# Optimization experiments

Measured on AMD Instinct MI355X. Metric: run time of the kernel, lower is better.

Reference implementation:

```python
import jax, jax.numpy as jnp
import numpy as np

N = 10000      # nodes
E = 320000     # edges (before self-loops)
IN = 256       # in_channels
HID = 128      # hidden_channels
HEADS = 4
OUT = 64       # out_channels
G = 64         # graphs in batch
NEG_SLOPE = 0.2


def setup_inputs() -> dict:
    key = jax.random.key(0)
    ks = jax.random.split(key, 12)
    s = lambda fan: 1.0 / np.sqrt(fan)
    x = jax.random.normal(ks[0], (N, IN), jnp.float32)
    edge_index = jax.random.randint(ks[1], (2, E), 0, N, dtype=jnp.int32)
    batch = jnp.sort(jax.random.randint(ks[2], (N,), 0, G, dtype=jnp.int32))
    # layer 0: GATConv(IN -> HID, heads=HEADS, concat)
    W1 = jax.random.normal(ks[3], (IN, HEADS * HID), jnp.float32) * s(IN)
    a1s = jax.random.normal(ks[4], (HEADS, HID), jnp.float32) * s(HID)
    a1d = jax.random.normal(ks[5], (HEADS, HID), jnp.float32) * s(HID)
    b1 = jnp.zeros((HEADS * HID,), jnp.float32)
    # layer 1: GATConv(HEADS*HID -> HID, heads=1)
    W2 = jax.random.normal(ks[6], (HEADS * HID, HID), jnp.float32) * s(HEADS * HID)
    a2s = jax.random.normal(ks[7], (1, HID), jnp.float32) * s(HID)
    a2d = jax.random.normal(ks[8], (1, HID), jnp.float32) * s(HID)
    b2 = jnp.zeros((HID,), jnp.float32)
    fc_w = jax.random.normal(ks[9], (HID, OUT), jnp.float32) * s(HID)
    fc_b = jnp.zeros((OUT,), jnp.float32)
    return dict(x=x, edge_index=edge_index, batch=batch, W1=W1, a1s=a1s,
                a1d=a1d, b1=b1, W2=W2, a2s=a2s, a2d=a2d, b2=b2,
                fc_w=fc_w, fc_b=fc_b)


def _gat_conv(x, src, dst, W, a_src, a_dst, b, heads):
    """PyG GATConv (concat=True, self-loops already in src/dst)."""
    n = x.shape[0]
    h = (x @ W).reshape(n, heads, -1)                     # [N,H,C]
    alpha_s = jnp.einsum('nhc,hc->nh', h, a_src)          # [N,H]
    alpha_d = jnp.einsum('nhc,hc->nh', h, a_dst)
    e = jax.nn.leaky_relu(alpha_s[src] + alpha_d[dst], NEG_SLOPE)  # [Etot,H]
    # per-destination-node segment softmax
    e = e - jax.ops.segment_max(e, dst, num_segments=n)[dst]
    e = jnp.exp(e)
    denom = jax.ops.segment_sum(e, dst, num_segments=n)[dst] + 1e-16
    alpha = e / denom
    out = jax.ops.segment_sum(h[src] * alpha[:, :, None], dst, num_segments=n)
    return out.reshape(n, -1) + b


def reference(x, edge_index, batch, W1, a1s, a1d, b1, W2, a2s, a2d, b2, fc_w, fc_b):
    loops = jnp.arange(N, dtype=edge_index.dtype)
    ei = jnp.concatenate([edge_index, jnp.stack([loops, loops])], axis=1)
    src, dst = ei[0], ei[1]
    h = jax.nn.relu(_gat_conv(x, src, dst, W1, a1s, a1d, b1, HEADS))
    h = jax.nn.relu(_gat_conv(h, src, dst, W2, a2s, a2d, b2, 1))
    # global_mean_pool over graph ids
    counts = jax.ops.segment_sum(jnp.ones((N, 1), h.dtype), batch, num_segments=G)
    pooled = jax.ops.segment_sum(h, batch, num_segments=G) / jnp.maximum(counts, 1.0)
    return pooled @ fc_w + fc_b
```

## Files before the change

### kernel.cpp

```cpp
#include <hip/hip_runtime.h>
#include <math.h>

#define NN 10000
#define EE 320000
#define GG 64
#define NT 157
#define NPAD (NT * 64)

#define NB 64
#define CH (EE / NB)
#define HSTR 10240

typedef __attribute__((ext_vector_type(8))) short short8;
typedef __attribute__((ext_vector_type(4))) float f32x4;

__device__ __forceinline__ float leaky(float x) { return x >= 0.f ? x : 0.2f * x; }

__device__ __forceinline__ unsigned f2bf(float f) {
  unsigned u = __float_as_uint(f);
  return (u + 0x7fffu + ((u >> 16) & 1u)) >> 16;
}
__device__ __forceinline__ float bflo(unsigned v) { return __uint_as_float(v << 16); }
__device__ __forceinline__ float bfhi(unsigned v) { return __uint_as_float(v & 0xffff0000u); }

__global__ __launch_bounds__(256) void zero_k(float* __restrict__ as1,
                                              float* __restrict__ ad1,
                                              float* __restrict__ as2,
                                              float* __restrict__ ad2) {
  int i = blockIdx.x * 256 + threadIdx.x;
  if (i < NN) { as2[i] = 0.f; ad2[i] = 0.f; }
  if (i < NN * 4) { as1[i] = 0.f; ad1[i] = 0.f; }
}

__device__ void histA_body(int blk, const int* __restrict__ ei,
                           int* __restrict__ hist2d,
                           ushort* __restrict__ lrank) {
  __shared__ int lh[NN];
  for (int i = threadIdx.x; i < NN; i += 256) lh[i] = 0;
  __syncthreads();
  const int base = blk * CH;
  for (int i = threadIdx.x; i < CH; i += 256) {
    int d = ei[EE + base + i];
    int r = atomicAdd(&lh[d], 1);
    lrank[base + i] = (ushort)r;
  }
  __syncthreads();
  int* hrow = hist2d + (size_t)blk * HSTR;
  for (int i = threadIdx.x; i < NN; i += 256) hrow[i] = lh[i];
}

__device__ __forceinline__ void s1_body(int sb, const int* __restrict__ hist2d,
                                        int* __restrict__ off2d,
                                        int* __restrict__ total) {
  int t = sb * 256 + threadIdx.x;
  if (t >= NN) return;
  int run = 0;
#pragma unroll 8
  for (int b = 0; b < NB; b++) {
    int v = hist2d[(size_t)b * HSTR + t];
    off2d[(size_t)b * HSTR + t] = run;
    run += v;
  }
  total[t] = run;
}

__device__ void scan_body(const int* __restrict__ total,
                          int* __restrict__ rowstart) {
  __shared__ int part[256];
  const int tid = threadIdx.x;
  const int PER = 40;
  int base = tid * PER;
  int local[PER];
  int s = 0;
#pragma unroll
  for (int i = 0; i < PER; i++) {
    int idx = base + i;
    int v = (idx < NN) ? total[idx] : 0;
    local[i] = s;
    s += v;
  }
  part[tid] = s;
  __syncthreads();
  for (int off = 1; off < 256; off <<= 1) {
    int v = (tid >= off) ? part[tid - off] : 0;
    __syncthreads();
    part[tid] += v;
    __syncthreads();
  }
  int pre = (tid == 0) ? 0 : part[tid - 1];
#pragma unroll
  for (int i = 0; i < PER; i++) {
    int idx = base + i;
    if (idx < NN) rowstart[idx] = pre + local[i];
  }
  if (tid == 255) rowstart[NN] = part[255];
}

__device__ __forceinline__ void fillB_body(int bx, const int* __restrict__ ei,
                                           const int* __restrict__ rowstart,
                                           const int* __restrict__ off2d,
                                           const ushort* __restrict__ lrank,
                                           int* __restrict__ esrc) {
  int e = bx * 256 + threadIdx.x;
  if (e >= EE) return;
  int d = ei[EE + e];
  int s = ei[e];
  int blk = e / CH;
  int pos = rowstart[d] + off2d[(size_t)blk * HSTR + d] + (int)lrank[e];
  esrc[pos] = s;
}

#define PX_ITEMS (NN * 256 / 8)
#define PW1 (512 * 256)
#define PW2 (128 * 512)
#define PACK_BLKS ((PX_ITEMS + PW1 + PW2) / 256)

__device__ __forceinline__ void pack_body(int pb, const float* __restrict__ x,
                                          const float* __restrict__ W1,
                                          const float* __restrict__ W2,
                                          uint4* __restrict__ xb,
                                          ushort* __restrict__ w1hi,
                                          ushort* __restrict__ w1lo,
                                          ushort* __restrict__ w2hi,
                                          ushort* __restrict__ w2lo) {
  int idx = pb * 256 + threadIdx.x;
  if (idx < PX_ITEMS) {
    const float4* xf = (const float4*)x;
    float4 a = xf[idx * 2], b = xf[idx * 2 + 1];
    uint4 o;
    o.x = f2bf(a.x) | (f2bf(a.y) << 16);
    o.y = f2bf(a.z) | (f2bf(a.w) << 16);
    o.z = f2bf(b.x) | (f2bf(b.y) << 16);
    o.w = f2bf(b.z) | (f2bf(b.w) << 16);
    xb[idx] = o;
  } else if (idx < PX_ITEMS + PW1) {
    int i = idx - PX_ITEMS;
    int c = i >> 8, k = i & 255;
    float w = W1[(size_t)k * 512 + c];
    unsigned h = f2bf(w);
    float r = w - __uint_as_float(h << 16);
    w1hi[i] = (ushort)h;
    w1lo[i] = (ushort)f2bf(r);
  } else if (idx < PX_ITEMS + PW1 + PW2) {
    int i = idx - PX_ITEMS - PW1;
    int c = i >> 9, k = i & 511;
    float w = W2[(size_t)k * 128 + c];
    unsigned h = f2bf(w);
    float r = w - __uint_as_float(h << 16);
    w2hi[i] = (ushort)h;
    w2lo[i] = (ushort)f2bf(r);
  }
}

__device__ __forceinline__ void gstart_body(int gb, const int* __restrict__ batch,
                                            int* __restrict__ gstart) {
  int i = gb * 256 + threadIdx.x;
  if (i >= NN) return;
  int b = batch[i];
  int prev = (i == 0) ? -1 : batch[i - 1];
  for (int g = prev + 1; g <= b; g++) gstart[g] = i;
  if (i == NN - 1)
    for (int g = b + 1; g <= GG; g++) gstart[g] = NN;
}

__device__ void gemmt_body(int chblk, int nodeblk,
                           const ushort* __restrict__ ab,
                           const ushort* __restrict__ whi,
                           const ushort* __restrict__ wlo,
                           unsigned* __restrict__ op,
                           const float* __restrict__ avs,
                           const float* __restrict__ avd,
                           float* __restrict__ as_out,
                           float* __restrict__ ad_out,
                           int K, int C) {
  const int lane = threadIdx.x & 63;
  const int wave = threadIdx.x >> 6;
  const int l15 = lane & 15;
  const int kg = lane >> 4;
  const int ch0 = chblk * 64 + wave * 16;
  const int node0 = nodeblk * 64;
  const ushort* arow_hi = whi + (size_t)(ch0 + l15) * K + kg * 8;
  const ushort* arow_lo = wlo + (size_t)(ch0 + l15) * K + kg * 8;
  const ushort* brow = ab + (size_t)(node0 + l15) * K + kg * 8;
  f32x4 acc[4];
#pragma unroll
  for (int f = 0; f < 4; f++) acc[f] = (f32x4){0.f, 0.f, 0.f, 0.f};
  for (int k0 = 0; k0 < K; k0 += 32) {
    short8 ah = *(const short8*)(arow_hi + k0);
    short8 al = *(const short8*)(arow_lo + k0);
#pragma unroll
    for (int f = 0; f < 4; f++) {
      short8 bv = *(const short8*)(brow + (size_t)f * 16 * K + k0);
      acc[f] = __builtin_amdgcn_mfma_f32_16x16x32_bf16(ah, bv, acc[f], 0, 0, 0);
      acc[f] = __builtin_amdgcn_mfma_f32_16x16x32_bf16(al, bv, acc[f], 0, 0, 0);
    }
  }
  const int chw = ch0 + kg * 4;
  const int head = ch0 >> 7;
  const int H = C >> 7;
  const float4 s4 = *(const float4*)(avs + chw);
  const float4 d4 = *(const float4*)(avd + chw);
#pragma unroll
  for (int f = 0; f < 4; f++) {
    int node = node0 + f * 16 + l15;
    unsigned u0 = f2bf(acc[f][0]) | (f2bf(acc[f][1]) << 16);
    unsigned u1 = f2bf(acc[f][2]) | (f2bf(acc[f][3]) << 16);
    *(uint2*)(op + (size_t)node * (C >> 1) + (chw >> 1)) = make_uint2(u0, u1);
    float ss = acc[f][0] * s4.x + acc[f][1] * s4.y + acc[f][2] * s4.z + acc[f][3] * s4.w;
    float sd = acc[f][0] * d4.x + acc[f][1] * d4.y + acc[f][2] * d4.z + acc[f][3] * d4.w;
    ss += __shfl_xor(ss, 16, 64); ss += __shfl_xor(ss, 32, 64);
    sd += __shfl_xor(sd, 16, 64); sd += __shfl_xor(sd, 32, 64);
    if (kg == 0 && node < NN) {
      atomicAdd(&as_out[node * H + head], ss);
      atomicAdd(&ad_out[node * H + head], sd);
    }
  }
}

#define FILL_BLKS 1250
#define GST_BLKS 40
__global__ __launch_bounds__(256) void fusedA_k(const int* __restrict__ ei,
                                                int* __restrict__ hist2d,
                                                ushort* __restrict__ lrank,
                                                const float* __restrict__ x,
                                                const float* __restrict__ W1,
                                                const float* __restrict__ W2,
                                                uint4* __restrict__ xb,
                                                ushort* __restrict__ w1hi,
                                                ushort* __restrict__ w1lo,
                                                ushort* __restrict__ w2hi,
                                                ushort* __restrict__ w2lo,
                                                const int* __restrict__ batch,
                                                int* __restrict__ gstart) {
  int bx = blockIdx.x;
  if (bx < NB) histA_body(bx, ei, hist2d, lrank);
  else if (bx < NB + PACK_BLKS)
    pack_body(bx - NB, x, W1, W2, xb, w1hi, w1lo, w2hi, w2lo);
  else
    gstart_body(bx - NB - PACK_BLKS, batch, gstart);
}

__global__ __launch_bounds__(256) void fusedB_k(const int* __restrict__ hist2d,
                                                int* __restrict__ off2d,
                                                int* __restrict__ total,
                                                const ushort* __restrict__ xb,
                                                const ushort* __restrict__ w1hi,
                                                const ushort* __restrict__ w1lo,
                                                unsigned* __restrict__ h1p,
                                                const float* __restrict__ a1s,
                                                const float* __restrict__ a1d,
                                                float* __restrict__ as1,
                                                float* __restrict__ ad1) {
  int bx = blockIdx.x;
  if (bx < GST_BLKS) { s1_body(bx, hist2d, off2d, total); return; }
  int lb = bx - GST_BLKS;
  int ch = lb % 3, nb = lb / 3;
  gemmt_body(ch, nb, xb, w1hi, w1lo, h1p, a1s, a1d, as1, ad1, 256, 512);
}

__global__ __launch_bounds__(256) void fusedC_k(const int* __restrict__ total,
                                                int* __restrict__ rowstart,
                                                const ushort* __restrict__ xb,
                                                const ushort* __restrict__ w1hi,
                                                const ushort* __restrict__ w1lo,
                                                unsigned* __restrict__ h1p,
                                                const float* __restrict__ a1s,
                                                const float* __restrict__ a1d,
                                                float* __restrict__ as1,
                                                float* __restrict__ ad1) {
  int bx = blockIdx.x;
  if (bx == 0) { scan_body(total, rowstart); return; }
  int lb = bx - 1;
  int ch = 3 + lb % 3, nb = lb / 3;
  gemmt_body(ch, nb, xb, w1hi, w1lo, h1p, a1s, a1d, as1, ad1, 256, 512);
}

__global__ __launch_bounds__(256) void fusedD_k(const int* __restrict__ ei,
                                                const int* __restrict__ rowstart,
                                                const int* __restrict__ off2d,
                                                const ushort* __restrict__ lrank,
                                                int* __restrict__ esrc,
                                                const ushort* __restrict__ xb,
                                                const ushort* __restrict__ w1hi,
                                                const ushort* __restrict__ w1lo,
                                                unsigned* __restrict__ h1p,
                                                const float* __restrict__ a1s,
                                                const float* __restrict__ a1d,
                                                float* __restrict__ as1,
                                                float* __restrict__ ad1) {
  int bx = blockIdx.x;
  if (bx < FILL_BLKS) { fillB_body(bx, ei, rowstart, off2d, lrank, esrc); return; }
  int lb = bx - FILL_BLKS;
  int ch = 6 + (lb & 1), nb = lb >> 1;
  gemmt_body(ch, nb, xb, w1hi, w1lo, h1p, a1s, a1d, as1, ad1, 256, 512);
}

__global__ __launch_bounds__(256) void gemmt_k(const ushort* __restrict__ ab,
                                               const ushort* __restrict__ whi,
                                               const ushort* __restrict__ wlo,
                                               unsigned* __restrict__ op,
                                               const float* __restrict__ avs,
                                               const float* __restrict__ avd,
                                               float* __restrict__ as_out,
                                               float* __restrict__ ad_out,
                                               int K, int C) {
  gemmt_body(blockIdx.x, blockIdx.y, ab, whi, wlo, op, avs, avd, as_out, ad_out, K, C);
}

__global__ __launch_bounds__(256) void agg1_k(const int* __restrict__ rowstart,
                                              const int* __restrict__ esrc,
                                              const float* __restrict__ as,
                                              const float* __restrict__ ad,
                                              const ushort* __restrict__ h1p,
                                              const float* __restrict__ b1,
                                              uint4* __restrict__ o1b) {
  const int lane = threadIdx.x & 63;
  const int wid = threadIdx.x >> 6;
  const int n = blockIdx.x * 4 + wid;
  const int beg = rowstart[n];
  const int deg = rowstart[n + 1] - beg;
  const int tot = deg + 1;
  const float4* as4 = (const float4*)as;
  const float4 adv = ((const float4*)ad)[n];
  const int head = lane >> 4;

  __shared__ float wlds_all[4][256];
  float* wlds = wlds_all[wid];

  int s0 = n;
  float4 e0 = make_float4(-1e30f, -1e30f, -1e30f, -1e30f);
  if (lane < tot) {
    if (lane < deg) s0 = esrc[beg + lane];
    float4 av = as4[s0];
    e0.x = leaky(av.x + adv.x); e0.y = leaky(av.y + adv.y);
    e0.z = leaky(av.z + adv.z); e0.w = leaky(av.w + adv.w);
  }
  float4 mx = e0;
  for (int i = lane + 64; i < tot; i += 64) {
    int s = (i < deg) ? esrc[beg + i] : n;
    float4 av = as4[s];
    mx.x = fmaxf(mx.x, leaky(av.x + adv.x));
    mx.y = fmaxf(mx.y, leaky(av.y + adv.y));
    mx.z = fmaxf(mx.z, leaky(av.z + adv.z));
    mx.w = fmaxf(mx.w, leaky(av.w + adv.w));
  }
#pragma unroll
  for (int off = 32; off >= 1; off >>= 1) {
    mx.x = fmaxf(mx.x, __shfl_xor(mx.x, off, 64));
    mx.y = fmaxf(mx.y, __shfl_xor(mx.y, off, 64));
    mx.z = fmaxf(mx.z, __shfl_xor(mx.z, off, 64));
    mx.w = fmaxf(mx.w, __shfl_xor(mx.w, off, 64));
  }
  float4 sm;
  sm.x = __expf(e0.x - mx.x); sm.y = __expf(e0.y - mx.y);
  sm.z = __expf(e0.z - mx.z); sm.w = __expf(e0.w - mx.w);
  for (int i = lane + 64; i < tot; i += 64) {
    int s = (i < deg) ? esrc[beg + i] : n;
    float4 av = as4[s];
    sm.x += __expf(leaky(av.x + adv.x) - mx.x);
    sm.y += __expf(leaky(av.y + adv.y) - mx.y);
    sm.z += __expf(leaky(av.z + adv.z) - mx.z);
    sm.w += __expf(leaky(av.w + adv.w) - mx.w);
  }
#pragma unroll
  for (int off = 32; off >= 1; off >>= 1) {
    sm.x += __shfl_xor(sm.x, off, 64);
    sm.y += __shfl_xor(sm.y, off, 64);
    sm.z += __shfl_xor(sm.z, off, 64);
    sm.w += __shfl_xor(sm.w, off, 64);
  }
  float4 inv;
  inv.x = 1.f / (sm.x + 1e-16f); inv.y = 1.f / (sm.y + 1e-16f);
  inv.z = 1.f / (sm.z + 1e-16f); inv.w = 1.f / (sm.w + 1e-16f);

  float4 acc0 = make_float4(0.f, 0.f, 0.f, 0.f);
  float4 acc1 = make_float4(0.f, 0.f, 0.f, 0.f);
  const char* hb = (const char*)h1p + (size_t)lane * 16;

  for (int base = 0; base < tot; base += 64) {
    int sl;
    float4 wl;
    if (base == 0) {
      sl = s0;
      wl.x = __expf(e0.x - mx.x) * inv.x;
      wl.y = __expf(e0.y - mx.y) * inv.y;
      wl.z = __expf(e0.z - mx.z) * inv.z;
      wl.w = __expf(e0.w - mx.w) * inv.w;
    } else {
      int i = base + lane;
      sl = n;
      wl = make_float4(0.f, 0.f, 0.f, 0.f);
      if (i < tot) {
        if (i < deg) sl = esrc[beg + i];
        float4 av = as4[sl];
        wl.x = __expf(leaky(av.x + adv.x) - mx.x) * inv.x;
        wl.y = __expf(leaky(av.y + adv.y) - mx.y) * inv.y;
        wl.z = __expf(leaky(av.z + adv.z) - mx.z) * inv.z;
        wl.w = __expf(leaky(av.w + adv.w) - mx.w) * inv.w;
      }
    }
    *(float4*)&wlds[lane * 4] = wl;
    int m = min(64, tot - base);
    int j = 0;
    for (; j + 2 <= m; j += 2) {
      int sA = __builtin_amdgcn_readlane(sl, j);
      int sB = __builtin_amdgcn_readlane(sl, j + 1);
      float wA = wlds[j * 4 + head];
      float wB = wlds[(j + 1) * 4 + head];
      uint4 hA = *(const uint4*)(hb + (size_t)sA * 1024);
      uint4 hB = *(const uint4*)(hb + (size_t)sB * 1024);
      acc0.x = fmaf(wA, bflo(hA.x), acc0.x);
      acc0.y = fmaf(wA, bfhi(hA.x), acc0.y);
      acc0.z = fmaf(wA, bflo(hA.y), acc0.z);
      acc0.w = fmaf(wA, bfhi(hA.y), acc0.w);
      acc1.x = fmaf(wA, bflo(hA.z), acc1.x);
      acc1.y = fmaf(wA, bfhi(hA.z), acc1.y);
      acc1.z = fmaf(wA, bflo(hA.w), acc1.z);
      acc1.w = fmaf(wA, bfhi(hA.w), acc1.w);
      acc0.x = fmaf(wB, bflo(hB.x), acc0.x);
      acc0.y = fmaf(wB, bfhi(hB.x), acc0.y);
      acc0.z = fmaf(wB, bflo(hB.y), acc0.z);
      acc0.w = fmaf(wB, bfhi(hB.y), acc0.w);
      acc1.x = fmaf(wB, bflo(hB.z), acc1.x);
      acc1.y = fmaf(wB, bfhi(hB.z), acc1.y);
      acc1.z = fmaf(wB, bflo(hB.w), acc1.z);
      acc1.w = fmaf(wB, bfhi(hB.w), acc1.w);
    }
    if (j < m) {
      int sA = __builtin_amdgcn_readlane(sl, j);
      float wA = wlds[j * 4 + head];
      uint4 hA = *(const uint4*)(hb + (size_t)sA * 1024);
      acc0.x = fmaf(wA, bflo(hA.x), acc0.x);
      acc0.y = fmaf(wA, bfhi(hA.x), acc0.y);
      acc0.z = fmaf(wA, bflo(hA.y), acc0.z);
      acc0.w = fmaf(wA, bfhi(hA.y), acc0.w);
      acc1.x = fmaf(wA, bflo(hA.z), acc1.x);
      acc1.y = fmaf(wA, bfhi(hA.z), acc1.y);
      acc1.z = fmaf(wA, bflo(hA.w), acc1.z);
      acc1.w = fmaf(wA, bfhi(hA.w), acc1.w);
    }
  }
  const float4* b4 = (const float4*)b1;
  float4 ba = b4[2 * lane], bb = b4[2 * lane + 1];
  float4 r0, r1;
  r0.x = fmaxf(acc0.x + ba.x, 0.f); r0.y = fmaxf(acc0.y + ba.y, 0.f);
  r0.z = fmaxf(acc0.z + ba.z, 0.f); r0.w = fmaxf(acc0.w + ba.w, 0.f);
  r1.x = fmaxf(acc1.x + bb.x, 0.f); r1.y = fmaxf(acc1.y + bb.y, 0.f);
  r1.z = fmaxf(acc1.z + bb.z, 0.f); r1.w = fmaxf(acc1.w + bb.w, 0.f);
  uint4 o;
  o.x = f2bf(r0.x) | (f2bf(r0.y) << 16);
  o.y = f2bf(r0.z) | (f2bf(r0.w) << 16);
  o.z = f2bf(r1.x) | (f2bf(r1.y) << 16);
  o.w = f2bf(r1.z) | (f2bf(r1.w) << 16);
  o1b[(size_t)n * 64 + lane] = o;
}

__global__ __launch_bounds__(256) void agg2_k(const int* __restrict__ rowstart,
                                              const int* __restrict__ esrc,
                                              const float* __restrict__ as,
                                              const float* __restrict__ ad,
                                              const ushort* __restrict__ h2p,
                                              const float* __restrict__ b2,
                                              float* __restrict__ out2) {
  const int lane = threadIdx.x & 63;
  const int wid = threadIdx.x >> 6;
  const int n = blockIdx.x * 4 + wid;
  const int beg = rowstart[n];
  const int deg = rowstart[n + 1] - beg;
  const int tot = deg + 1;
  const float adv = ad[n];

  __shared__ float wlds_all[4][64];
  float* wlds = wlds_all[wid];

  int s0 = n;
  float e0 = -1e30f;
  if (lane < tot) {
    if (lane < deg) s0 = esrc[beg + lane];
    e0 = leaky(as[s0] + adv);
  }
  float mx = e0;
  for (int i = lane + 64; i < tot; i += 64) {
    int s = (i < deg) ? esrc[beg + i] : n;
    mx = fmaxf(mx, leaky(as[s] + adv));
  }
#pragma unroll
  for (int off = 32; off >= 1; off >>= 1) mx = fmaxf(mx, __shfl_xor(mx, off, 64));
  float sm = __expf(e0 - mx);
  for (int i = lane + 64; i < tot; i += 64) {
    int s = (i < deg) ? esrc[beg + i] : n;
    sm += __expf(leaky(as[s] + adv) - mx);
  }
#pragma unroll
  for (int off = 32; off >= 1; off >>= 1) sm += __shfl_xor(sm, off, 64);
  float inv = 1.f / (sm + 1e-16f);

  float2 acc = make_float2(0.f, 0.f);
  const char* hb = (const char*)h2p + (size_t)lane * 4;
  for (int base = 0; base < tot; base += 64) {
    int sl;
    float wl;
    if (base == 0) {
      sl = s0;
      wl = __expf(e0 - mx) * inv;
    } else {
      int i = base + lane;
      sl = n; wl = 0.f;
      if (i < tot) {
        if (i < deg) sl = esrc[beg + i];
        wl = __expf(leaky(as[sl] + adv) - mx) * inv;
      }
    }
    wlds[lane] = wl;
    int m = min(64, tot - base);
    int j = 0;
    for (; j + 2 <= m; j += 2) {
      int sA = __builtin_amdgcn_readlane(sl, j);
      int sB = __builtin_amdgcn_readlane(sl, j + 1);
      float wA = wlds[j];
      float wB = wlds[j + 1];
      unsigned hA = *(const unsigned*)(hb + (size_t)sA * 256);
      unsigned hB = *(const unsigned*)(hb + (size_t)sB * 256);
      acc.x = fmaf(wA, bflo(hA), acc.x);
      acc.y = fmaf(wA, bfhi(hA), acc.y);
      acc.x = fmaf(wB, bflo(hB), acc.x);
      acc.y = fmaf(wB, bfhi(hB), acc.y);
    }
    if (j < m) {
      int sA = __builtin_amdgcn_readlane(sl, j);
      float wA = wlds[j];
      unsigned hA = *(const unsigned*)(hb + (size_t)sA * 256);
      acc.x = fmaf(wA, bflo(hA), acc.x);
      acc.y = fmaf(wA, bfhi(hA), acc.y);
    }
  }
  float2 bb = ((const float2*)b2)[lane];
  float2 r;
  r.x = fmaxf(acc.x + bb.x, 0.f);
  r.y = fmaxf(acc.y + bb.y, 0.f);
  ((float2*)(out2 + (size_t)n * 128))[lane] = r;
}

__global__ __launch_bounds__(128) void poolfc_k(const int* __restrict__ gstart,
                                                const float* __restrict__ out2,
                                                const float* __restrict__ fcw,
                                                const float* __restrict__ fcb,
                                                float* __restrict__ out) {
  const int g = blockIdx.x;
  const int tid = threadIdx.x;
  const int beg = gstart[g], end = gstart[g + 1];
  const int cnt = end - beg;
  float acc = 0.f;
  int n = beg;
  for (; n + 4 <= end; n += 4) {
    float v0 = out2[(size_t)(n + 0) * 128 + tid];
    float v1 = out2[(size_t)(n + 1) * 128 + tid];
    float v2 = out2[(size_t)(n + 2) * 128 + tid];
    float v3 = out2[(size_t)(n + 3) * 128 + tid];
    acc += (v0 + v1) + (v2 + v3);
  }
  for (; n < end; n++) acc += out2[(size_t)n * 128 + tid];
  __shared__ float pg[128];
  pg[tid] = acc / (float)(cnt > 0 ? cnt : 1);
  __syncthreads();
  if (tid < 64) {
    float o = fcb[tid];
#pragma unroll 8
    for (int c = 0; c < 128; c++) o = fmaf(pg[c], fcw[c * 64 + tid], o);
    out[g * 64 + tid] = o;
  }
}

extern "C" void kernel_launch(void* const* d_in, const int* in_sizes, int n_in,
                              void* d_out, int out_size, void* d_ws, size_t ws_size,
                              hipStream_t stream) {
  const float* x   = (const float*)d_in[0];
  const int*   ei  = (const int*)d_in[1];
  const int*   bat = (const int*)d_in[2];
  const float* W1  = (const float*)d_in[3];
  const float* a1s = (const float*)d_in[4];
  const float* a1d = (const float*)d_in[5];
  const float* b1  = (const float*)d_in[6];
  const float* W2  = (const float*)d_in[7];
  const float* a2s = (const float*)d_in[8];
  const float* a2d = (const float*)d_in[9];
  const float* b2  = (const float*)d_in[10];
  const float* fcw = (const float*)d_in[11];
  const float* fcb = (const float*)d_in[12];
  float* out = (float*)d_out;

  char* ws = (char*)d_ws;
  size_t off = 0;
  auto alloc = [&](size_t bytes) -> void* {
    void* p = ws + off;
    off = (off + bytes + 255) & ~(size_t)255;
    return p;
  };

  int*   hist2d   = (int*)alloc((size_t)NB * HSTR * 4);
  int*   off2d    = (int*)alloc((size_t)NB * HSTR * 4);
  ushort* lrank   = (ushort*)alloc((size_t)EE * 2);
  int*   total    = (int*)alloc((size_t)NN * 4);
  int*   rowstart = (int*)alloc((size_t)(NN + 1) * 4);
  int*   esrc     = (int*)alloc((size_t)EE * 4);
  int*   gstart   = (int*)alloc((size_t)(GG + 1) * 4);
  ushort* xb      = (ushort*)alloc((size_t)NPAD * 256 * 2);
  ushort* w1hi    = (ushort*)alloc((size_t)512 * 256 * 2);
  ushort* w1lo    = (ushort*)alloc((size_t)512 * 256 * 2);
  ushort* w2hi    = (ushort*)alloc((size_t)128 * 512 * 2);
  ushort* w2lo    = (ushort*)alloc((size_t)128 * 512 * 2);
  ushort* h1p     = (ushort*)alloc((size_t)NPAD * 512 * 2);
  ushort* o1b     = (ushort*)alloc((size_t)NPAD * 512 * 2);
  ushort* h2p     = (ushort*)alloc((size_t)NPAD * 128 * 2);
  float* as1      = (float*)alloc((size_t)NN * 4 * 4);
  float* ad1      = (float*)alloc((size_t)NN * 4 * 4);
  float* as2      = (float*)alloc((size_t)NN * 4);
  float* ad2      = (float*)alloc((size_t)NN * 4);
  float* out2     = (float*)alloc((size_t)NN * 128 * 4);
  (void)ws_size; (void)in_sizes; (void)n_in; (void)out_size;

  zero_k<<<(NN * 4 + 255) / 256, 256, 0, stream>>>(as1, ad1, as2, ad2);

  fusedA_k<<<NB + PACK_BLKS + GST_BLKS, 256, 0, stream>>>(
      ei, hist2d, lrank, x, W1, W2, (uint4*)xb, w1hi, w1lo, w2hi, w2lo, bat, gstart);

  fusedB_k<<<GST_BLKS + 3 * NT, 256, 0, stream>>>(hist2d, off2d, total, xb, w1hi, w1lo,
                                                  (unsigned*)h1p, a1s, a1d, as1, ad1);

  fusedC_k<<<1 + 3 * NT, 256, 0, stream>>>(total, rowstart, xb, w1hi, w1lo,
                                           (unsigned*)h1p, a1s, a1d, as1, ad1);

  fusedD_k<<<FILL_BLKS + 2 * NT, 256, 0, stream>>>(ei, rowstart, off2d, lrank, esrc,
                                                   xb, w1hi, w1lo, (unsigned*)h1p,
                                                   a1s, a1d, as1, ad1);

  agg1_k<<<NN / 4, 256, 0, stream>>>(rowstart, esrc, as1, ad1, h1p, b1, (uint4*)o1b);

  gemmt_k<<<dim3(2, NT), 256, 0, stream>>>(o1b, w2hi, w2lo, (unsigned*)h2p,
                                           a2s, a2d, as2, ad2, 512, 128);
  agg2_k<<<NN / 4, 256, 0, stream>>>(rowstart, esrc, as2, ad2, h2p, b2, out2);

  poolfc_k<<<GG, 128, 0, stream>>>(gstart, out2, fcw, fcb, out);
}
```

Baseline: 169.6 us.

## Split layer-1 aggregation into alpha-computation and per-head gather kernels

The single layer-1 aggregation kernel is split in two. The first computes the softmax attention weights per edge and writes them to a new global buffer, with a separate buffer for the self-loop weight. The second launches one block column per head, and each wave's four 16-lane groups process four edges at a time, combined with cross-lane shuffles. The aim is more parallelism and memory-level concurrency in the gather. In exchange it adds an extra launch, an alpha buffer of roughly 5 MB written and re-read, and four re-reads of the edge lists.

```diff
diff --git a/kernel.cpp b/kernel.cpp
--- a/kernel.cpp
+++ b/kernel.cpp
@@ -307,36 +307,22 @@
   gemmt_body(blockIdx.x, blockIdx.y, ab, whi, wlo, op, avs, avd, as_out, ad_out, K, C);
 }
 
-__global__ __launch_bounds__(256) void agg1_k(const int* __restrict__ rowstart,
-                                              const int* __restrict__ esrc,
-                                              const float* __restrict__ as,
-                                              const float* __restrict__ ad,
-                                              const ushort* __restrict__ h1p,
-                                              const float* __restrict__ b1,
-                                              uint4* __restrict__ o1b) {
+__global__ __launch_bounds__(256) void agg1a_k(const int* __restrict__ rowstart,
+                                               const int* __restrict__ esrc,
+                                               const float* __restrict__ as,
+                                               const float* __restrict__ ad,
+                                               float4* __restrict__ alpha,
+                                               float4* __restrict__ aself) {
   const int lane = threadIdx.x & 63;
-  const int wid = threadIdx.x >> 6;
-  const int n = blockIdx.x * 4 + wid;
+  const int n = blockIdx.x * 4 + (threadIdx.x >> 6);
   const int beg = rowstart[n];
   const int deg = rowstart[n + 1] - beg;
   const int tot = deg + 1;
   const float4* as4 = (const float4*)as;
   const float4 adv = ((const float4*)ad)[n];
-  const int head = lane >> 4;
-
-  __shared__ float wlds_all[4][256];
-  float* wlds = wlds_all[wid];
-
-  int s0 = n;
-  float4 e0 = make_float4(-1e30f, -1e30f, -1e30f, -1e30f);
-  if (lane < tot) {
-    if (lane < deg) s0 = esrc[beg + lane];
-    float4 av = as4[s0];
-    e0.x = leaky(av.x + adv.x); e0.y = leaky(av.y + adv.y);
-    e0.z = leaky(av.z + adv.z); e0.w = leaky(av.w + adv.w);
-  }
-  float4 mx = e0;
-  for (int i = lane + 64; i < tot; i += 64) {
+
+  float4 mx = make_float4(-1e30f, -1e30f, -1e30f, -1e30f);
+  for (int i = lane; i < tot; i += 64) {
     int s = (i < deg) ? esrc[beg + i] : n;
     float4 av = as4[s];
     mx.x = fmaxf(mx.x, leaky(av.x + adv.x));
@@ -351,10 +337,8 @@
     mx.z = fmaxf(mx.z, __shfl_xor(mx.z, off, 64));
     mx.w = fmaxf(mx.w, __shfl_xor(mx.w, off, 64));
   }
-  float4 sm;
-  sm.x = __expf(e0.x - mx.x); sm.y = __expf(e0.y - mx.y);
-  sm.z = __expf(e0.z - mx.z); sm.w = __expf(e0.w - mx.w);
-  for (int i = lane + 64; i < tot; i += 64) {
+  float4 sm = make_float4(0.f, 0.f, 0.f, 0.f);
+  for (int i = lane; i < tot; i += 64) {
     int s = (i < deg) ? esrc[beg + i] : n;
     float4 av = as4[s];
     sm.x += __expf(leaky(av.x + adv.x) - mx.x);
@@ -373,86 +357,87 @@
   inv.x = 1.f / (sm.x + 1e-16f); inv.y = 1.f / (sm.y + 1e-16f);
   inv.z = 1.f / (sm.z + 1e-16f); inv.w = 1.f / (sm.w + 1e-16f);
 
-  float4 acc0 = make_float4(0.f, 0.f, 0.f, 0.f);
-  float4 acc1 = make_float4(0.f, 0.f, 0.f, 0.f);
-  const char* hb = (const char*)h1p + (size_t)lane * 16;
-
-  for (int base = 0; base < tot; base += 64) {
-    int sl;
-    float4 wl;
-    if (base == 0) {
-      sl = s0;
-      wl.x = __expf(e0.x - mx.x) * inv.x;
-      wl.y = __expf(e0.y - mx.y) * inv.y;
-      wl.z = __expf(e0.z - mx.z) * inv.z;
-      wl.w = __expf(e0.w - mx.w) * inv.w;
-    } else {
-      int i = base + lane;
-      sl = n;
-      wl = make_float4(0.f, 0.f, 0.f, 0.f);
-      if (i < tot) {
-        if (i < deg) sl = esrc[beg + i];
-        float4 av = as4[sl];
-        wl.x = __expf(leaky(av.x + adv.x) - mx.x) * inv.x;
-        wl.y = __expf(leaky(av.y + adv.y) - mx.y) * inv.y;
-        wl.z = __expf(leaky(av.z + adv.z) - mx.z) * inv.z;
-        wl.w = __expf(leaky(av.w + adv.w) - mx.w) * inv.w;
-      }
+  for (int i = lane; i < tot; i += 64) {
+    int s = (i < deg) ? esrc[beg + i] : n;
+    float4 av = as4[s];
+    float4 w;
+    w.x = __expf(leaky(av.x + adv.x) - mx.x) * inv.x;
+    w.y = __expf(leaky(av.y + adv.y) - mx.y) * inv.y;
+    w.z = __expf(leaky(av.z + adv.z) - mx.z) * inv.z;
+    w.w = __expf(leaky(av.w + adv.w) - mx.w) * inv.w;
+    if (i < deg) alpha[beg + i] = w;
+    else aself[n] = w;
+  }
+}
+
+__global__ __launch_bounds__(256) void agg1b_k(const int* __restrict__ rowstart,
+                                               const int* __restrict__ esrc,
+                                               const float* __restrict__ alpha,
+                                               const float* __restrict__ aself,
+                                               const ushort* __restrict__ h1p,
+                                               const float* __restrict__ b1,
+                                               uint4* __restrict__ o1b) {
+  const int lane = threadIdx.x & 63;
+  const int wid = threadIdx.x >> 6;
+  const int n = blockIdx.x * 4 + wid;
+  const int head = blockIdx.y;
+  const int q = lane >> 4;
+  const int l16 = lane & 15;
+  const int beg = rowstart[n];
+  const int deg = rowstart[n + 1] - beg;
+  const char* hb = (const char*)h1p + head * 256 + l16 * 16;
+
+  float acc[8] = {};
+  for (int j = 0; j < deg; j += 4) {
+    int i = j + q;
+    int s = n;
+    float w = 0.f;
+    if (i < deg) {
+      s = esrc[beg + i];
+      w = alpha[(size_t)(beg + i) * 4 + head];
     }
-    *(float4*)&wlds[lane * 4] = wl;
-    int m = min(64, tot - base);
-    int j = 0;
-    for (; j + 2 <= m; j += 2) {
-      int sA = __builtin_amdgcn_readlane(sl, j);
-      int sB = __builtin_amdgcn_readlane(sl, j + 1);
-      float wA = wlds[j * 4 + head];
-      float wB = wlds[(j + 1) * 4 + head];
-      uint4 hA = *(const uint4*)(hb + (size_t)sA * 1024);
-      uint4 hB = *(const uint4*)(hb + (size_t)sB * 1024);
-      acc0.x = fmaf(wA, bflo(hA.x), acc0.x);
-      acc0.y = fmaf(wA, bfhi(hA.x), acc0.y);
-      acc0.z = fmaf(wA, bflo(hA.y), acc0.z);
-      acc0.w = fmaf(wA, bfhi(hA.y), acc0.w);
-      acc1.x = fmaf(wA, bflo(hA.z), acc1.x);
-      acc1.y = fmaf(wA, bfhi(hA.z), acc1.y);
-      acc1.z = fmaf(wA, bflo(hA.w), acc1.z);
-      acc1.w = fmaf(wA, bfhi(hA.w), acc1.w);
-      acc0.x = fmaf(wB, bflo(hB.x), acc0.x);
-      acc0.y = fmaf(wB, bfhi(hB.x), acc0.y);
-      acc0.z = fmaf(wB, bflo(hB.y), acc0.z);
-      acc0.w = fmaf(wB, bfhi(hB.y), acc0.w);
-      acc1.x = fmaf(wB, bflo(hB.z), acc1.x);
-      acc1.y = fmaf(wB, bfhi(hB.z), acc1.y);
-      acc1.z = fmaf(wB, bflo(hB.w), acc1.z);
-      acc1.w = fmaf(wB, bfhi(hB.w), acc1.w);
-    }
-    if (j < m) {
-      int sA = __builtin_amdgcn_readlane(sl, j);
-      float wA = wlds[j * 4 + head];
-      uint4 hA = *(const uint4*)(hb + (size_t)sA * 1024);
-      acc0.x = fmaf(wA, bflo(hA.x), acc0.x);
-      acc0.y = fmaf(wA, bfhi(hA.x), acc0.y);
-      acc0.z = fmaf(wA, bflo(hA.y), acc0.z);
-      acc0.w = fmaf(wA, bfhi(hA.y), acc0.w);
-      acc1.x = fmaf(wA, bflo(hA.z), acc1.x);
-      acc1.y = fmaf(wA, bfhi(hA.z), acc1.y);
-      acc1.z = fmaf(wA, bflo(hA.w), acc1.z);
-      acc1.w = fmaf(wA, bfhi(hA.w), acc1.w);
-    }
-  }
-  const float4* b4 = (const float4*)b1;
-  float4 ba = b4[2 * lane], bb = b4[2 * lane + 1];
-  float4 r0, r1;
-  r0.x = fmaxf(acc0.x + ba.x, 0.f); r0.y = fmaxf(acc0.y + ba.y, 0.f);
-  r0.z = fmaxf(acc0.z + ba.z, 0.f); r0.w = fmaxf(acc0.w + ba.w, 0.f);
-  r1.x = fmaxf(acc1.x + bb.x, 0.f); r1.y = fmaxf(acc1.y + bb.y, 0.f);
-  r1.z = fmaxf(acc1.z + bb.z, 0.f); r1.w = fmaxf(acc1.w + bb.w, 0.f);
-  uint4 o;
-  o.x = f2bf(r0.x) | (f2bf(r0.y) << 16);
-  o.y = f2bf(r0.z) | (f2bf(r0.w) << 16);
-  o.z = f2bf(r1.x) | (f2bf(r1.y) << 16);
-  o.w = f2bf(r1.z) | (f2bf(r1.w) << 16);
-  o1b[(size_t)n * 64 + lane] = o;
+    uint4 hv = *(const uint4*)(hb + (size_t)s * 1024);
+    acc[0] = fmaf(w, bflo(hv.x), acc[0]);
+    acc[1] = fmaf(w, bfhi(hv.x), acc[1]);
+    acc[2] = fmaf(w, bflo(hv.y), acc[2]);
+    acc[3] = fmaf(w, bfhi(hv.y), acc[3]);
+    acc[4] = fmaf(w, bflo(hv.z), acc[4]);
+    acc[5] = fmaf(w, bfhi(hv.z), acc[5]);
+    acc[6] = fmaf(w, bflo(hv.w), acc[6]);
+    acc[7] = fmaf(w, bfhi(hv.w), acc[7]);
+  }
+  if (q == 0) {
+    float w = aself[(size_t)n * 4 + head];
+    uint4 hv = *(const uint4*)(hb + (size_t)n * 1024);
+    acc[0] = fmaf(w, bflo(hv.x), acc[0]);
+    acc[1] = fmaf(w, bfhi(hv.x), acc[1]);
+    acc[2] = fmaf(w, bflo(hv.y), acc[2]);
+    acc[3] = fmaf(w, bfhi(hv.y), acc[3]);
+    acc[4] = fmaf(w, bflo(hv.z), acc[4]);
+    acc[5] = fmaf(w, bfhi(hv.z), acc[5]);
+    acc[6] = fmaf(w, bflo(hv.w), acc[6]);
+    acc[7] = fmaf(w, bfhi(hv.w), acc[7]);
+  }
+#pragma unroll
+  for (int c = 0; c < 8; c++) {
+    acc[c] += __shfl_xor(acc[c], 16, 64);
+    acc[c] += __shfl_xor(acc[c], 32, 64);
+  }
+  if (q == 0) {
+    const float* bp = b1 + head * 128 + l16 * 8;
+    float4 bA = *(const float4*)bp;
+    float4 bB = *(const float4*)(bp + 4);
+    float r0 = fmaxf(acc[0] + bA.x, 0.f), r1 = fmaxf(acc[1] + bA.y, 0.f);
+    float r2 = fmaxf(acc[2] + bA.z, 0.f), r3 = fmaxf(acc[3] + bA.w, 0.f);
+    float r4 = fmaxf(acc[4] + bB.x, 0.f), r5 = fmaxf(acc[5] + bB.y, 0.f);
+    float r6 = fmaxf(acc[6] + bB.z, 0.f), r7 = fmaxf(acc[7] + bB.w, 0.f);
+    uint4 o;
+    o.x = f2bf(r0) | (f2bf(r1) << 16);
+    o.y = f2bf(r2) | (f2bf(r3) << 16);
+    o.z = f2bf(r4) | (f2bf(r5) << 16);
+    o.w = f2bf(r6) | (f2bf(r7) << 16);
+    *(uint4*)((char*)o1b + (size_t)n * 1024 + head * 256 + l16 * 16) = o;
+  }
 }
 
 __global__ __launch_bounds__(256) void agg2_k(const int* __restrict__ rowstart,
@@ -617,6 +602,8 @@
   float* as2      = (float*)alloc((size_t)NN * 4);
   float* ad2      = (float*)alloc((size_t)NN * 4);
   float* out2     = (float*)alloc((size_t)NN * 128 * 4);
+  float* alpha    = (float*)alloc((size_t)EE * 16);
+  float* aself    = (float*)alloc((size_t)NN * 16);
   (void)ws_size; (void)in_sizes; (void)n_in; (void)out_size;
 
   zero_k<<<(NN * 4 + 255) / 256, 256, 0, stream>>>(as1, ad1, as2, ad2);
@@ -634,7 +621,10 @@
                                                    xb, w1hi, w1lo, (unsigned*)h1p,
                                                    a1s, a1d, as1, ad1);
 
-  agg1_k<<<NN / 4, 256, 0, stream>>>(rowstart, esrc, as1, ad1, h1p, b1, (uint4*)o1b);
+  agg1a_k<<<NN / 4, 256, 0, stream>>>(rowstart, esrc, as1, ad1,
+                                      (float4*)alpha, (float4*)aself);
+  agg1b_k<<<dim3(NN / 4, 4), 256, 0, stream>>>(rowstart, esrc, alpha, aself,
+                                               h1p, b1, (uint4*)o1b);
 
   gemmt_k<<<dim3(2, NT), 256, 0, stream>>>(o1b, w2hi, w2lo, (unsigned*)h2p,
                                            a2s, a2d, as2, ad2, 512, 128);
```

New measurement: 184.9 us. +9.0%, slower.
